# Performance work log

Measured on AMD Instinct MI355X. Metric: run time of the kernel, lower is better.

The kernel has to match this reference:

```python
import jax, jax.numpy as jnp
import numpy as np

H, W, C = 64, 64, 2048
IMG = 224


def setup_inputs() -> dict:
    key = jax.random.key(0)
    features = jax.random.normal(key, (2, H, W, C), dtype=jnp.float32)
    return {"features": features, "img_size": IMG}


def reference(features, img_size):
    # features: [2, H, W, C] -- query (index 0) and target (index 1) feature maps.
    x0 = features[0]  # [H, W, C]
    x1 = features[1]  # [H, W, C]
    # Correlation volume: Decomposition[i,j,k,l] = sum_c x0[i,j,c] * x1[k,l,c]
    # (replaces the quadruple Python loop with a single GEMM-shaped einsum)
    decom = jnp.einsum('ijc,klc->ijkl', x0, x1)  # [H, W, H, W]
    decom = decom / jnp.max(decom)
    # NOTE: source calls `Decomposition.clamp(min=0)` without assignment -> no-op.
    decom_1 = jnp.sum(decom, axis=(2, 3))  # [H, W] saliency on query image
    decom_2 = jnp.sum(decom, axis=(0, 1))  # [H, W] saliency on target image
    stacked = jnp.stack((decom_1, decom_2))  # [2, H, W]
    # F.interpolate(mode='bilinear', align_corners=False) == half-pixel bilinear resize
    out = jax.image.resize(stacked, (2, img_size, img_size), method='bilinear')
    return out  # [2, img_size, img_size]
```

## Files before the change

kernel.cpp:

```cpp
#include <hip/hip_runtime.h>
#include <hip/hip_bf16.h>

#define HW    4096
#define CDIM  2048
#define IMG   224
#define NTKI  64
#define NTM   128
#define LROW  528
#define QSCALE 21.166666f
#define NS    32
#define SBUF3 32768

typedef int   int4v  __attribute__((ext_vector_type(4)));
typedef int   i32x16 __attribute__((ext_vector_type(16)));
typedef char  char4v __attribute__((ext_vector_type(4)));

__device__ __forceinline__ i32x16 zi16() {
    i32x16 z;
#pragma unroll
    for (int i = 0; i < 16; ++i) z[i] = 0;
    return z;
}
__device__ __forceinline__ char quant8(float x) {
    int r = __float2int_rn(x * QSCALE);
    r = min(max(r, -127), 127);
    return (char)r;
}

__device__ __forceinline__ void gload_lds16(const char* g, char* l) {
    __builtin_amdgcn_global_load_lds(
        (const __attribute__((address_space(1))) void*)g,
        (__attribute__((address_space(3))) void*)l, 16, 0, 0);
}

__global__ __launch_bounds__(256) void convert_pack_partial(
    const float* __restrict__ feat,
    char* __restrict__ Ap, char* __restrict__ Bp,
    float* __restrict__ P) {
    __shared__ char lds[64 * LROW];
    __shared__ float csum[512];
    const int tid = threadIdx.x;
    const int mat = blockIdx.z;
    const int rm  = blockIdx.y;
    const int kb0 = blockIdx.x * 512;
    const float* src = feat + (size_t)mat * HW * CDIM + (size_t)(rm * 64) * CDIM + kb0;

    const int cc = (tid & 127) * 4;
    float a0 = 0.f, a1 = 0.f, a2 = 0.f, a3 = 0.f;
#pragma unroll
    for (int j = 0; j < 32; ++j) {
        const int r = j * 2 + (tid >> 7);
        float4 v = *(const float4*)&src[(size_t)r * CDIM + cc];
        a0 += v.x; a1 += v.y; a2 += v.z; a3 += v.w;
        char4v q;
        q[0] = quant8(v.x); q[1] = quant8(v.y);
        q[2] = quant8(v.z); q[3] = quant8(v.w);
        *(char4v*)&lds[r * LROW + cc] = q;
    }
    if (tid >= 128) {
        csum[cc + 0] = a0; csum[cc + 1] = a1;
        csum[cc + 2] = a2; csum[cc + 3] = a3;
    }
    __syncthreads();
    if (tid < 128) {
        float4 p;
        p.x = a0 + csum[cc + 0]; p.y = a1 + csum[cc + 1];
        p.z = a2 + csum[cc + 2]; p.w = a3 + csum[cc + 3];
        *(float4*)&P[((size_t)mat * 64 + rm) * CDIM + kb0 + cc] = p;
    }

    const int l = tid & 63, w = tid >> 6;
    char* dstbase = mat ? Bp : Ap;
#pragma unroll
    for (int i = 0; i < 8; ++i) {
        const int t = w * 8 + i;
        const int tml = t >> 4, tkl = t & 15;
        int4v v = *(const int4v*)
            &lds[(tml * 32 + (l & 31)) * LROW + tkl * 32 + (l >> 5) * 16];
        const int tm  = rm * 2 + tml;
        const int tkg = blockIdx.x * 16 + tkl;
        *(int4v*)&dstbase[((size_t)(tm * NTKI + tkg) * 64 + l) * 16] = v;
    }
}

__global__ __launch_bounds__(256, 1) void gemm_max_kernel(
    const char* __restrict__ Ap, const char* __restrict__ Bp,
    const float* __restrict__ P, float* __restrict__ s,
    float* __restrict__ blockmax) {
    __shared__ char lds[3 * SBUF3];
    __shared__ int wred[4];
    const int tid  = threadIdx.x;
    const int lane = tid & 63;
    const int wave = tid >> 6;
    const int wm = wave >> 1, wn = wave & 1;

    const int bid = blockIdx.y * gridDim.x + blockIdx.x;
    const int xcd = bid & 7;
    const int wix = bid >> 3;
    const int bm  = (xcd >> 2) * 8 + (wix >> 2);
    const int bn  = (xcd & 3) * 4 + (wix & 3);

    const char* gb[8];
    int loff[8];
#pragma unroll
    for (int q = 0; q < 8; ++q) {
        const int c = wave * 8 + q;
        const int kk = c & 1;
        if (c < 16) {
            const int il = c >> 1;
            gb[q] = Ap + ((size_t)(bm * 8 + il) * NTKI + kk) * 1024 + lane * 16;
            loff[q] = il * 2048 + kk * 1024;
        } else {
            const int jl = (c - 16) >> 1;
            gb[q] = Bp + ((size_t)(bn * 8 + jl) * NTKI + kk) * 1024 + lane * 16;
            loff[q] = 16384 + jl * 2048 + kk * 1024;
        }
    }

#define ISSUE_STAGE(S, BUF) do {                                    \
        _Pragma("unroll")                                           \
        for (int q = 0; q < 8; ++q)                                 \
            gload_lds16(gb[q] + (size_t)(S) * 2048, (BUF) + loff[q]);\
    } while (0)

    char* r0 = lds;
    char* r1 = lds + SBUF3;
    char* r2 = lds + 2 * SBUF3;

    ISSUE_STAGE(0, r0); ISSUE_STAGE(1, r1);

    if (bm == 15) {
        const int gc = bn * 256 + tid;
        const float* Pp = P + (size_t)(gc >> 11) * 64 * CDIM + (gc & 2047);
        float sum = 0.f;
#pragma unroll 8
        for (int r = 0; r < 64; ++r) sum += Pp[(size_t)r * CDIM];
        s[gc] = sum;
    }

    asm volatile("s_waitcnt vmcnt(8)" ::: "memory");
    asm volatile("s_barrier" ::: "memory");

    const int aoff = wm * 8192 + lane * 16;
    const int boff = 16384 + wn * 8192 + lane * 16;

    i32x16 acc[4][4];
#pragma unroll
    for (int i = 0; i < 4; ++i)
#pragma unroll
        for (int j = 0; j < 4; ++j) {
            acc[i][j] = zi16();
            asm volatile("" : "+a"(acc[i][j]));
        }

#define READ_HALF(AR, BR, BASE, KK) do {                                    \
        _Pragma("unroll")                                                   \
        for (int i = 0; i < 4; ++i)                                         \
            AR[i][KK] = *(const int4v*)((BASE) + aoff + i * 2048 + (KK) * 1024); \
        _Pragma("unroll")                                                   \
        for (int j = 0; j < 4; ++j)                                         \
            BR[j][KK] = *(const int4v*)((BASE) + boff + j * 2048 + (KK) * 1024); \
    } while (0)

#define MFMA_HALF(AR, BR, KK) do {                                          \
        __builtin_amdgcn_s_setprio(1);                                      \
        _Pragma("unroll")                                                   \
        for (int i = 0; i < 4; ++i)                                         \
            _Pragma("unroll")                                               \
            for (int j = 0; j < 4; ++j)                                     \
                acc[i][j] = __builtin_amdgcn_mfma_i32_32x32x32_i8(          \
                    AR[i][KK], BR[j][KK], acc[i][j], 0, 0, 0);              \
        __builtin_amdgcn_s_setprio(0);                                      \
    } while (0)

#define ROTATE() do { char* t_ = r0; r0 = r1; r1 = r2; r2 = t_; } while (0)

    int4v xa[4][2], xb[4][2];
    int4v ya[4][2], yb[4][2];

    READ_HALF(xa, xb, r0, 0);
    READ_HALF(xa, xb, r0, 1);

    for (int it = 0; it < 16; ++it) {
        if (it < 15) {
            ISSUE_STAGE(2 * it + 2, r2);
            asm volatile("s_waitcnt vmcnt(8)" ::: "memory");
        } else {
            asm volatile("s_waitcnt vmcnt(0)" ::: "memory");
        }
        asm volatile("s_barrier" ::: "memory");
        READ_HALF(ya, yb, r1, 0);
        MFMA_HALF(xa, xb, 0);
        READ_HALF(ya, yb, r1, 1);
        MFMA_HALF(xa, xb, 1);
        ROTATE();

        if (it < 15) {
            ISSUE_STAGE(2 * it + 3, r2);
            asm volatile("s_waitcnt vmcnt(8)" ::: "memory");
        } else {
            asm volatile("s_waitcnt vmcnt(0)" ::: "memory");
        }
        asm volatile("s_barrier" ::: "memory");
        READ_HALF(xa, xb, r1, 0);
        MFMA_HALF(ya, yb, 0);
        READ_HALF(xa, xb, r1, 1);
        MFMA_HALF(ya, yb, 1);
        ROTATE();
    }
#undef ISSUE_STAGE
#undef READ_HALF
#undef MFMA_HALF
#undef ROTATE

    int m = INT_MIN;
#pragma unroll
    for (int i = 0; i < 4; ++i)
#pragma unroll
        for (int j = 0; j < 4; ++j)
#pragma unroll
            for (int e = 0; e < 16; ++e)
                m = max(m, acc[i][j][e]);
#pragma unroll
    for (int off = 32; off; off >>= 1)
        m = max(m, __shfl_down(m, off));
    if (lane == 0) wred[wave] = m;
    __syncthreads();
    if (tid == 0) {
        const int im = max(max(wred[0], wred[1]), max(wred[2], wred[3]));
        blockmax[bid] = (float)im * (1.0f / (QSCALE * QSCALE));
    }
}

__global__ __launch_bounds__(256) void saliency_kernel(
    const float* __restrict__ feat, const float* __restrict__ s,
    float* __restrict__ sal) {
    const int tid = threadIdx.x, lane = tid & 63, wave = tid >> 6;
    const int g = blockIdx.x * 4 + wave;
    const float* x;
    const float* sv;
    if (g < HW) { x = feat + (size_t)g * CDIM;                            sv = s + CDIM; }
    else        { x = feat + (size_t)HW * CDIM + (size_t)(g - HW) * CDIM; sv = s; }
    float acc = 0.f;
#pragma unroll
    for (int it = 0; it < 8; ++it) {
        const int c0 = it * 256 + lane * 4;
        float4 v = *(const float4*)&x[c0];
        float4 w = *(const float4*)&sv[c0];
        acc += v.x * w.x + v.y * w.y + v.z * w.z + v.w * w.w;
    }
#pragma unroll
    for (int off = 32; off; off >>= 1) acc += __shfl_down(acc, off);
    if (lane == 0) sal[g] = acc;
}

__global__ __launch_bounds__(256) void resize_kernel(
    const float* __restrict__ sal, const float* __restrict__ bmax,
    float* __restrict__ out) {
    __shared__ float w[4];
    __shared__ float rM;
    const int tid = threadIdx.x;
    float m = -3.4e38f;
    for (int i = tid; i < 256; i += 256) m = fmaxf(m, bmax[i]);
#pragma unroll
    for (int off = 32; off; off >>= 1) m = fmaxf(m, __shfl_down(m, off));
    if ((tid & 63) == 0) w[tid >> 6] = m;
    __syncthreads();
    if (tid == 0)
        rM = 1.0f / fmaxf(fmaxf(w[0], w[1]), fmaxf(w[2], w[3]));
    __syncthreads();

    const int idx = blockIdx.x * 256 + tid;
    if (idx >= 2 * IMG * IMG) return;
    const int ch = idx / (IMG * IMG);
    const int rem = idx % (IMG * IMG);
    const int oy = rem / IMG, ox = rem % IMG;
    const float scale = 64.0f / (float)IMG;
    const float sy = ((float)oy + 0.5f) * scale - 0.5f;
    const float sx = ((float)ox + 0.5f) * scale - 0.5f;
    const float fy0 = floorf(sy), fx0 = floorf(sx);
    const float wy = sy - fy0, wx = sx - fx0;
    int y0 = (int)fy0, x0 = (int)fx0;
    int y1 = min(max(y0 + 1, 0), 63), x1 = min(max(x0 + 1, 0), 63);
    y0 = min(max(y0, 0), 63); x0 = min(max(x0, 0), 63);
    const float* p = sal + ch * HW;
    const float v00 = p[y0 * 64 + x0], v01 = p[y0 * 64 + x1];
    const float v10 = p[y1 * 64 + x0], v11 = p[y1 * 64 + x1];
    out[idx] = ((1.f - wy) * ((1.f - wx) * v00 + wx * v01) +
                wy * ((1.f - wx) * v10 + wx * v11)) * rM;
}

extern "C" void kernel_launch(void* const* d_in, const int* in_sizes, int n_in,
                              void* d_out, int out_size, void* d_ws, size_t ws_size,
                              hipStream_t stream) {
    const float* feat = (const float*)d_in[0];
    float* out = (float*)d_out;

    char* ws = (char*)d_ws;
    char* Ap = ws;
    char* Bp = ws + (size_t)8 * 1024 * 1024;
    float* P    = (float*)(ws + (size_t)16 * 1024 * 1024);
    float* s    = P + 2 * 64 * CDIM;
    float* bmax = s + 2 * CDIM;
    float* sal  = bmax + 1024;

    convert_pack_partial<<<dim3(4, 64, 2), 256, 0, stream>>>(feat, Ap, Bp, P);
    gemm_max_kernel<<<dim3(16, 16), 256, 0, stream>>>(Ap, Bp, P, s, bmax);
    saliency_kernel<<<2048, 256, 0, stream>>>(feat, s, sal);
    const int nout = 2 * IMG * IMG;
    resize_kernel<<<(nout + 255) / 256, 256, 0, stream>>>(sal, bmax, out);
}
```

Measured before the change: 138.5 us.

## Halve convert tile rows and reduce column sums with atomics instead of GEMM pass

The convert/pack kernel now processes 32-row tiles instead of 64, doubling its grid to 1024 blocks for better occupancy. Column sums are accumulated directly into the final sum vector with float atomicAdd after a memset, replacing the partial-sum buffer. This removes the extra reduction the GEMM kernel's last block-row performed. The cost is an extra memset launch and atomic contention across 128 row tiles per column, and the float atomics make summation order nondeterministic.

```diff
diff --git a/kernel.cpp b/kernel.cpp
--- a/kernel.cpp
+++ b/kernel.cpp
@@ -33,22 +33,22 @@
         (__attribute__((address_space(3))) void*)l, 16, 0, 0);
 }
 
-__global__ __launch_bounds__(256) void convert_pack_partial(
+__global__ __launch_bounds__(256) void convert_pack(
     const float* __restrict__ feat,
     char* __restrict__ Ap, char* __restrict__ Bp,
-    float* __restrict__ P) {
-    __shared__ char lds[64 * LROW];
+    float* __restrict__ s) {
+    __shared__ char lds[32 * LROW];
     __shared__ float csum[512];
     const int tid = threadIdx.x;
     const int mat = blockIdx.z;
-    const int rm  = blockIdx.y;
+    const int rt  = blockIdx.y;
     const int kb0 = blockIdx.x * 512;
-    const float* src = feat + (size_t)mat * HW * CDIM + (size_t)(rm * 64) * CDIM + kb0;
+    const float* src = feat + (size_t)mat * HW * CDIM + (size_t)(rt * 32) * CDIM + kb0;
 
     const int cc = (tid & 127) * 4;
     float a0 = 0.f, a1 = 0.f, a2 = 0.f, a3 = 0.f;
 #pragma unroll
-    for (int j = 0; j < 32; ++j) {
+    for (int j = 0; j < 16; ++j) {
         const int r = j * 2 + (tid >> 7);
         float4 v = *(const float4*)&src[(size_t)r * CDIM + cc];
         a0 += v.x; a1 += v.y; a2 += v.z; a3 += v.w;
@@ -63,29 +63,27 @@
     }
     __syncthreads();
     if (tid < 128) {
-        float4 p;
-        p.x = a0 + csum[cc + 0]; p.y = a1 + csum[cc + 1];
-        p.z = a2 + csum[cc + 2]; p.w = a3 + csum[cc + 3];
-        *(float4*)&P[((size_t)mat * 64 + rm) * CDIM + kb0 + cc] = p;
+        float* sp = s + (size_t)mat * CDIM + kb0 + cc;
+        atomicAdd(sp + 0, a0 + csum[cc + 0]);
+        atomicAdd(sp + 1, a1 + csum[cc + 1]);
+        atomicAdd(sp + 2, a2 + csum[cc + 2]);
+        atomicAdd(sp + 3, a3 + csum[cc + 3]);
     }
 
     const int l = tid & 63, w = tid >> 6;
     char* dstbase = mat ? Bp : Ap;
 #pragma unroll
-    for (int i = 0; i < 8; ++i) {
-        const int t = w * 8 + i;
-        const int tml = t >> 4, tkl = t & 15;
+    for (int i = 0; i < 4; ++i) {
+        const int tkl = w * 4 + i;
         int4v v = *(const int4v*)
-            &lds[(tml * 32 + (l & 31)) * LROW + tkl * 32 + (l >> 5) * 16];
-        const int tm  = rm * 2 + tml;
+            &lds[(l & 31) * LROW + tkl * 32 + (l >> 5) * 16];
         const int tkg = blockIdx.x * 16 + tkl;
-        *(int4v*)&dstbase[((size_t)(tm * NTKI + tkg) * 64 + l) * 16] = v;
+        *(int4v*)&dstbase[((size_t)(rt * NTKI + tkg) * 64 + l) * 16] = v;
     }
 }
 
 __global__ __launch_bounds__(256, 1) void gemm_max_kernel(
     const char* __restrict__ Ap, const char* __restrict__ Bp,
-    const float* __restrict__ P, float* __restrict__ s,
     float* __restrict__ blockmax) {
     __shared__ char lds[3 * SBUF3];
     __shared__ int wred[4];
@@ -128,15 +126,6 @@
     char* r2 = lds + 2 * SBUF3;
 
     ISSUE_STAGE(0, r0); ISSUE_STAGE(1, r1);
-
-    if (bm == 15) {
-        const int gc = bn * 256 + tid;
-        const float* Pp = P + (size_t)(gc >> 11) * 64 * CDIM + (gc & 2047);
-        float sum = 0.f;
-#pragma unroll 8
-        for (int r = 0; r < 64; ++r) sum += Pp[(size_t)r * CDIM];
-        s[gc] = sum;
-    }
 
     asm volatile("s_waitcnt vmcnt(8)" ::: "memory");
     asm volatile("s_barrier" ::: "memory");
@@ -299,13 +288,13 @@
     char* ws = (char*)d_ws;
     char* Ap = ws;
     char* Bp = ws + (size_t)8 * 1024 * 1024;
-    float* P    = (float*)(ws + (size_t)16 * 1024 * 1024);
-    float* s    = P + 2 * 64 * CDIM;
+    float* s    = (float*)(ws + (size_t)16 * 1024 * 1024);
     float* bmax = s + 2 * CDIM;
     float* sal  = bmax + 1024;
 
-    convert_pack_partial<<<dim3(4, 64, 2), 256, 0, stream>>>(feat, Ap, Bp, P);
-    gemm_max_kernel<<<dim3(16, 16), 256, 0, stream>>>(Ap, Bp, P, s, bmax);
+    hipMemsetAsync(s, 0, (size_t)2 * CDIM * sizeof(float), stream);
+    convert_pack<<<dim3(4, 128, 2), 256, 0, stream>>>(feat, Ap, Bp, s);
+    gemm_max_kernel<<<dim3(16, 16), 256, 0, stream>>>(Ap, Bp, bmax);
     saliency_kernel<<<2048, 256, 0, stream>>>(feat, s, sal);
     const int nout = 2 * IMG * IMG;
     resize_kernel<<<(nout + 255) / 256, 256, 0, stream>>>(sal, bmax, out);
```

After: 154.0 us. +11.2%, slower.
